# Kernel optimization log

Hardware: AMD Instinct MI355X
Metric: run time of the kernel (lower is better)

The kernel has to match this reference:

```python
import jax, jax.numpy as jnp
import numpy as np

B, D, H, V, T = 64, 1024, 1024, 32000, 20
SOS = 0  # word_to_idx['<SOS>']


def setup_inputs() -> dict:
    key = jax.random.key(0)
    ks = jax.random.split(key, 6)
    s = 0.02
    return {
        "latent_vector": jax.random.normal(ks[0], (B, D), jnp.float32),
        "W_proj": jax.random.normal(ks[1], (H, D), jnp.float32) * s,
        "b_proj": jnp.zeros((H,), jnp.float32),
        "emb": jax.random.normal(ks[2], (V, H), jnp.float32) * s,
        "W_ih": jax.random.normal(ks[3], (3 * H, H), jnp.float32) * s,
        "b_ih": jnp.zeros((3 * H,), jnp.float32),
        "W_hh": jax.random.normal(ks[4], (3 * H, H), jnp.float32) * s,
        "b_hh": jnp.zeros((3 * H,), jnp.float32),
        "W_out": jax.random.normal(ks[5], (V, H), jnp.float32) * s,
        "b_out": jnp.zeros((V,), jnp.float32),
    }


def _gru_cell(x, h, W_ih, b_ih, W_hh, b_hh):
    # PyTorch GRU cell gate math
    gi = x @ W_ih.T + b_ih  # [B, 3H]
    gh = h @ W_hh.T + b_hh  # [B, 3H]
    i_r, i_z, i_n = jnp.split(gi, 3, axis=-1)
    h_r, h_z, h_n = jnp.split(gh, 3, axis=-1)
    r = jax.nn.sigmoid(i_r + h_r)
    z = jax.nn.sigmoid(i_z + h_z)
    n = jnp.tanh(i_n + r * h_n)
    return (1.0 - z) * n + z * h


def reference(latent_vector, W_proj, b_proj, emb, W_ih, b_ih, W_hh, b_hh, W_out, b_out):
    batch = latent_vector.shape[0]
    h = latent_vector @ W_proj.T + b_proj  # init_hidden: [B, H]
    tok0 = jnp.full((batch,), SOS, dtype=jnp.int32)

    def step(carry, _):
        tok, h = carry
        x = emb[tok]                                  # embedding lookup [B, H]
        h = _gru_cell(x, h, W_ih, b_ih, W_hh, b_hh)   # GRU step
        logits = h @ W_out.T + b_out                  # [B, V]
        tok = jnp.argmax(logits, axis=-1).astype(jnp.int32)  # topk(1) greedy
        return (tok, h), tok

    (_, h_final), toks = jax.lax.scan(step, (tok0, h), None, length=T)
    # torch: stack(outputs, dim=1).squeeze() -> [B, T]; hidden -> [1, B, H]
    return toks.T, h_final[None, :, :]
```

## Files before the change

### kernel.cpp

```cpp
#include <hip/hip_runtime.h>
#include <stdint.h>

#define B_ 64
#define D_ 1024
#define H_ 1024
#define V_ 32000
#define T_ 20
#define SOS_ 0

typedef __attribute__((ext_vector_type(8))) __bf16 bf16x8;
typedef __attribute__((ext_vector_type(4))) float f32x4;

__device__ __forceinline__ uint32_t ord_of_float(float x) {
    uint32_t u = __float_as_uint(x);
    return (u & 0x80000000u) ? ~u : (u | 0x80000000u);
}

__device__ __forceinline__ unsigned long long shfl_xor_u64(unsigned long long x, int m) {
    return (unsigned long long)__shfl_xor((long long)x, m, 64);
}

__device__ __forceinline__ void split_bf16(float f, unsigned short* hi, unsigned short* lo) {
    uint32_t u = __float_as_uint(f);
    uint32_t rh = (u + 0x7FFFu + ((u >> 16) & 1u)) >> 16;
    *hi = (unsigned short)rh;
    float fl = f - __uint_as_float(rh << 16);
    uint32_t ul = __float_as_uint(fl);
    uint32_t rl = (ul + 0x7FFFu + ((ul >> 16) & 1u)) >> 16;
    *lo = (unsigned short)rl;
}

__device__ __forceinline__ void gload_lds16(const void* g, void* l) {
    __builtin_amdgcn_global_load_lds(
        (const __attribute__((address_space(1))) void*)g,
        (__attribute__((address_space(3))) void*)l, 16, 0, 0);
}

__global__ __launch_bounds__(256) void k_split_w(const float* __restrict__ src,
    unsigned short* __restrict__ hi, unsigned short* __restrict__ lo, int n4)
{
    int i = blockIdx.x * 256 + threadIdx.x;
    if (i >= n4) return;
    float4 v = ((const float4*)src)[i];
    ushort4 h, l;
    split_bf16(v.x, &h.x, &l.x);
    split_bf16(v.y, &h.y, &l.y);
    split_bf16(v.z, &h.z, &l.z);
    split_bf16(v.w, &h.w, &l.w);
    ((ushort4*)hi)[i] = h;
    ((ushort4*)lo)[i] = l;
}

__global__ __launch_bounds__(256) void k_init_hidden(
    const float* __restrict__ latent, const float* __restrict__ Wp,
    const float* __restrict__ bp, float* __restrict__ h0,
    unsigned short* __restrict__ hhi, unsigned short* __restrict__ hlo)
{
    int gw = (blockIdx.x * 256 + threadIdx.x) >> 6;
    int lane = threadIdx.x & 63;
    int j = gw >> 6;
    int b = gw & 63;
    const float4* a4 = (const float4*)(latent + b * D_);
    const float4* w4 = (const float4*)(Wp + (size_t)j * D_);
    float s = 0.f;
#pragma unroll
    for (int i = 0; i < 4; i++) {
        float4 a = a4[lane + 64 * i];
        float4 w = w4[lane + 64 * i];
        s += a.x * w.x + a.y * w.y + a.z * w.z + a.w * w.w;
    }
#pragma unroll
    for (int off = 32; off; off >>= 1) s += __shfl_down(s, off, 64);
    if (lane == 0) {
        float v = s + bp[j];
        h0[b * H_ + j] = v;
        unsigned short h_, l_;
        split_bf16(v, &h_, &l_);
        hhi[b * H_ + j] = h_;
        hlo[b * H_ + j] = l_;
    }
}

__global__ __launch_bounds__(256) void k_prep_x0(const float* __restrict__ emb,
    unsigned short* __restrict__ xhi, unsigned short* __restrict__ xlo)
{
    int b = blockIdx.x;
    int tid = threadIdx.x;
    float4 v4 = *(const float4*)(emb + (size_t)SOS_ * H_ + tid * 4);
    ushort4 h, l;
    split_bf16(v4.x, &h.x, &l.x);
    split_bf16(v4.y, &h.y, &l.y);
    split_bf16(v4.z, &h.z, &l.z);
    split_bf16(v4.w, &h.w, &l.w);
    *(ushort4*)(xhi + (size_t)b * H_ + tid * 4) = h;
    *(ushort4*)(xlo + (size_t)b * H_ + tid * 4) = l;
}

__global__ __launch_bounds__(256) void k_gates_gemm2(
    const unsigned short* __restrict__ xhi, const unsigned short* __restrict__ xlo,
    const unsigned short* __restrict__ hhi, const unsigned short* __restrict__ hlo,
    const unsigned short* __restrict__ wihh, const unsigned short* __restrict__ wihl,
    const unsigned short* __restrict__ whhh, const unsigned short* __restrict__ whhl,
    float* __restrict__ gbuf)
{
    __shared__ __align__(128) char Bsm[2][16384];
    int tid = threadIdx.x;
    int lane = tid & 63;
    int wv = tid >> 6;
    int blk = blockIdx.x;
    int jt = blk % 48;
    int rest = blk / 48;
    int half = rest & 1;
    int ks = rest >> 1;
    int kbase = ks * 512;
    int row0 = jt * 64;

    const unsigned short* Ahi_g = half ? hhi : xhi;
    const unsigned short* Alo_g = half ? hlo : xlo;
    const unsigned short* Bhi_g = half ? whhh : wihh;
    const unsigned short* Blo_g = half ? whhl : wihl;

    int r0 = wv * 8 + (lane >> 3);
    int r1 = r0 + 32;
    int kslt = (lane & 7) * 16;
    size_t so0 = (size_t)(row0 + r0) * 2048 + (size_t)(kslt ^ ((r0 & 7) << 4));
    size_t so1 = (size_t)(row0 + r1) * 2048 + (size_t)(kslt ^ ((r1 & 7) << 4));

    int mrow = wv * 16 + (lane & 15);
    int koff = (lane >> 4) * 8;
    int kb = koff * 2;

    f32x4 acc[4];
#pragma unroll
    for (int i = 0; i < 4; i++) acc[i] = (f32x4){0.f, 0.f, 0.f, 0.f};

    auto stage = [&](int BUF, int KC) {
        const char* bh = (const char*)Bhi_g + (size_t)KC * 2;
        const char* bl = (const char*)Blo_g + (size_t)KC * 2;
        char* base = Bsm[BUF] + wv * 1024;
        gload_lds16(bh + so0, base);
        gload_lds16(bh + so1, base + 4096);
        gload_lds16(bl + so0, base + 8192);
        gload_lds16(bl + so1, base + 12288);
    };

    int buf = 0;
    stage(0, kbase);
    __syncthreads();
    for (int it = 0; it < 8; ++it) {
        int kc = kbase + it * 64;
        if (it < 7) stage(buf ^ 1, kc + 64);
        const unsigned short* ap = Ahi_g + (size_t)mrow * 1024 + kc + koff;
        const unsigned short* alp = Alo_g + (size_t)mrow * 1024 + kc + koff;
        bf16x8 ah0 = *(const bf16x8*)ap;
        bf16x8 ah1 = *(const bf16x8*)(ap + 32);
        bf16x8 al0 = *(const bf16x8*)alp;
        bf16x8 al1 = *(const bf16x8*)(alp + 32);
        const char* bhp = Bsm[buf];
        const char* blp = Bsm[buf] + 8192;
#pragma unroll
        for (int tv = 0; tv < 4; tv++) {
            int brow = tv * 16 + (lane & 15);
            int swz = (brow & 7) << 4;
            int ro = brow * 128;
            bf16x8 bh0 = *(const bf16x8*)(bhp + ro + (kb ^ swz));
            bf16x8 bh1 = *(const bf16x8*)(bhp + ro + ((kb + 64) ^ swz));
            bf16x8 bl0 = *(const bf16x8*)(blp + ro + (kb ^ swz));
            bf16x8 bl1 = *(const bf16x8*)(blp + ro + ((kb + 64) ^ swz));
            acc[tv] = __builtin_amdgcn_mfma_f32_16x16x32_bf16(ah0, bh0, acc[tv], 0, 0, 0);
            acc[tv] = __builtin_amdgcn_mfma_f32_16x16x32_bf16(ah1, bh1, acc[tv], 0, 0, 0);
            acc[tv] = __builtin_amdgcn_mfma_f32_16x16x32_bf16(al0, bh0, acc[tv], 0, 0, 0);
            acc[tv] = __builtin_amdgcn_mfma_f32_16x16x32_bf16(al1, bh1, acc[tv], 0, 0, 0);
            acc[tv] = __builtin_amdgcn_mfma_f32_16x16x32_bf16(ah0, bl0, acc[tv], 0, 0, 0);
            acc[tv] = __builtin_amdgcn_mfma_f32_16x16x32_bf16(ah1, bl1, acc[tv], 0, 0, 0);
        }
        __syncthreads();
        buf ^= 1;
    }

    int col = lane & 15;
    int quad = lane >> 4;
    float* og = gbuf + (size_t)((ks * 2 + half) * 64) * 3072;
#pragma unroll
    for (int tv = 0; tv < 4; tv++) {
#pragma unroll
        for (int r = 0; r < 4; r++) {
            int b = wv * 16 + quad * 4 + r;
            og[(size_t)b * 3072 + jt * 64 + tv * 16 + col] = acc[tv][r];
        }
    }
}

__global__ __launch_bounds__(256) void k_gru_elem2(
    const float* __restrict__ gbuf, const float* __restrict__ bih,
    const float* __restrict__ bhh, const float* __restrict__ hprev,
    float* __restrict__ hnext, unsigned short* __restrict__ hnhi,
    unsigned short* __restrict__ hnlo)
{
    int idx = blockIdx.x * 256 + threadIdx.x;
    int b = idx >> 10;
    int j = idx & 1023;
    const float* g00 = gbuf + (size_t)b * 3072;
    const float* g01 = gbuf + (size_t)(64 + b) * 3072;
    const float* g10 = gbuf + (size_t)(128 + b) * 3072;
    const float* g11 = gbuf + (size_t)(192 + b) * 3072;
    float ir = g00[j] + g10[j] + bih[j];
    float hr = g01[j] + g11[j] + bhh[j];
    float iz = g00[H_ + j] + g10[H_ + j] + bih[H_ + j];
    float hz = g01[H_ + j] + g11[H_ + j] + bhh[H_ + j];
    float in_ = g00[2 * H_ + j] + g10[2 * H_ + j] + bih[2 * H_ + j];
    float hn = g01[2 * H_ + j] + g11[2 * H_ + j] + bhh[2 * H_ + j];
    float r = 1.f / (1.f + expf(-(ir + hr)));
    float z = 1.f / (1.f + expf(-(iz + hz)));
    float n = tanhf(in_ + r * hn);
    float hp = hprev[idx];
    float v = (1.f - z) * n + z * hp;
    hnext[idx] = v;
    unsigned short h_, l_;
    split_bf16(v, &h_, &l_);
    hnhi[idx] = h_;
    hnlo[idx] = l_;
}

__global__ __launch_bounds__(256) void k_logits_argmax2(
    const unsigned short* __restrict__ hhi, const unsigned short* __restrict__ hlo,
    const unsigned short* __restrict__ wouth, const unsigned short* __restrict__ woutl,
    const float* __restrict__ bout, unsigned long long* __restrict__ partials,
    int nblk)
{
    __shared__ __align__(128) char Bsm[2][16384];
    int tid = threadIdx.x;
    int lane = tid & 63;
    int wv = tid >> 6;
    int row0 = blockIdx.x * 64;

    int r0 = wv * 8 + (lane >> 3);
    int r1 = r0 + 32;
    int kslt = (lane & 7) * 16;
    size_t so0 = (size_t)(row0 + r0) * 2048 + (size_t)(kslt ^ ((r0 & 7) << 4));
    size_t so1 = (size_t)(row0 + r1) * 2048 + (size_t)(kslt ^ ((r1 & 7) << 4));

    int mrow = wv * 16 + (lane & 15);
    int koff = (lane >> 4) * 8;
    int kb = koff * 2;

    f32x4 acc[4];
#pragma unroll
    for (int i = 0; i < 4; i++) acc[i] = (f32x4){0.f, 0.f, 0.f, 0.f};

    auto stage = [&](int BUF, int KC) {
        const char* bh = (const char*)wouth + (size_t)KC * 2;
        const char* bl = (const char*)woutl + (size_t)KC * 2;
        char* base = Bsm[BUF] + wv * 1024;
        gload_lds16(bh + so0, base);
        gload_lds16(bh + so1, base + 4096);
        gload_lds16(bl + so0, base + 8192);
        gload_lds16(bl + so1, base + 12288);
    };

    int buf = 0;
    stage(0, 0);
    __syncthreads();
    for (int it = 0; it < 16; ++it) {
        int kc = it * 64;
        if (it < 15) stage(buf ^ 1, kc + 64);
        const unsigned short* ap = hhi + (size_t)mrow * 1024 + kc + koff;
        const unsigned short* alp = hlo + (size_t)mrow * 1024 + kc + koff;
        bf16x8 ah0 = *(const bf16x8*)ap;
        bf16x8 ah1 = *(const bf16x8*)(ap + 32);
        bf16x8 al0 = *(const bf16x8*)alp;
        bf16x8 al1 = *(const bf16x8*)(alp + 32);
        const char* bhp = Bsm[buf];
        const char* blp = Bsm[buf] + 8192;
#pragma unroll
        for (int tv = 0; tv < 4; tv++) {
            int brow = tv * 16 + (lane & 15);
            int swz = (brow & 7) << 4;
            int ro = brow * 128;
            bf16x8 bh0 = *(const bf16x8*)(bhp + ro + (kb ^ swz));
            bf16x8 bh1 = *(const bf16x8*)(bhp + ro + ((kb + 64) ^ swz));
            bf16x8 bl0 = *(const bf16x8*)(blp + ro + (kb ^ swz));
            bf16x8 bl1 = *(const bf16x8*)(blp + ro + ((kb + 64) ^ swz));
            acc[tv] = __builtin_amdgcn_mfma_f32_16x16x32_bf16(ah0, bh0, acc[tv], 0, 0, 0);
            acc[tv] = __builtin_amdgcn_mfma_f32_16x16x32_bf16(ah1, bh1, acc[tv], 0, 0, 0);
            acc[tv] = __builtin_amdgcn_mfma_f32_16x16x32_bf16(al0, bh0, acc[tv], 0, 0, 0);
            acc[tv] = __builtin_amdgcn_mfma_f32_16x16x32_bf16(al1, bh1, acc[tv], 0, 0, 0);
            acc[tv] = __builtin_amdgcn_mfma_f32_16x16x32_bf16(ah0, bl0, acc[tv], 0, 0, 0);
            acc[tv] = __builtin_amdgcn_mfma_f32_16x16x32_bf16(ah1, bl1, acc[tv], 0, 0, 0);
        }
        __syncthreads();
        buf ^= 1;
    }

    int col = lane & 15;
    int quad = lane >> 4;
    unsigned long long kmax[4] = {0ull, 0ull, 0ull, 0ull};
#pragma unroll
    for (int tv = 0; tv < 4; tv++) {
        int v = row0 + tv * 16 + col;
        float bo = bout[v];
#pragma unroll
        for (int r = 0; r < 4; r++) {
            float lg = acc[tv][r] + bo;
            unsigned long long key = ((unsigned long long)ord_of_float(lg) << 32)
                                   | (unsigned long long)(0x7FFFFFFFu - (uint32_t)v);
            if (key > kmax[r]) kmax[r] = key;
        }
    }
#pragma unroll
    for (int r = 0; r < 4; r++) {
        unsigned long long k = kmax[r];
#pragma unroll
        for (int off = 1; off < 16; off <<= 1) {
            unsigned long long o = shfl_xor_u64(k, off);
            if (o > k) k = o;
        }
        kmax[r] = k;
    }
    if (col == 0) {
#pragma unroll
        for (int r = 0; r < 4; r++) {
            int b = wv * 16 + quad * 4 + r;
            partials[(size_t)b * nblk + blockIdx.x] = kmax[r];
        }
    }
}

__global__ __launch_bounds__(256) void k_token2(
    const unsigned long long* __restrict__ partials, int nblk,
    int* __restrict__ tok, float* __restrict__ out_tokens, int t,
    const float* __restrict__ emb,
    unsigned short* __restrict__ xhi, unsigned short* __restrict__ xlo)
{
    __shared__ int s_tok;
    int b = blockIdx.x;
    int tid = threadIdx.x;
    if (tid < 64) {
        unsigned long long k = 0ull;
        for (int i = tid; i < nblk; i += 64) {
            unsigned long long p = partials[(size_t)b * nblk + i];
            if (p > k) k = p;
        }
#pragma unroll
        for (int off = 32; off; off >>= 1) {
            unsigned long long o = shfl_xor_u64(k, off);
            if (o > k) k = o;
        }
        if (tid == 0) {
            int v = (int)(0x7FFFFFFFu - (uint32_t)(k & 0xFFFFFFFFull));
            tok[b] = v;
            out_tokens[b * T_ + t] = (float)v;
            s_tok = v;
        }
    }
    __syncthreads();
    int row = s_tok;
    float4 v4 = *(const float4*)(emb + (size_t)row * H_ + tid * 4);
    ushort4 h, l;
    split_bf16(v4.x, &h.x, &l.x);
    split_bf16(v4.y, &h.y, &l.y);
    split_bf16(v4.z, &h.z, &l.z);
    split_bf16(v4.w, &h.w, &l.w);
    *(ushort4*)(xhi + (size_t)b * H_ + tid * 4) = h;
    *(ushort4*)(xlo + (size_t)b * H_ + tid * 4) = l;
}

__global__ __launch_bounds__(256) void k_copy_h(const float* __restrict__ h,
                                               float* __restrict__ out)
{
    int i = (blockIdx.x * 256 + threadIdx.x) * 4;
    *(float4*)(out + i) = *(const float4*)(h + i);
}

extern "C" void kernel_launch(void* const* d_in, const int* in_sizes, int n_in,
                              void* d_out, int out_size, void* d_ws, size_t ws_size,
                              hipStream_t stream)
{
    const float* latent = (const float*)d_in[0];
    const float* Wp     = (const float*)d_in[1];
    const float* bp     = (const float*)d_in[2];
    const float* emb    = (const float*)d_in[3];
    const float* Wih    = (const float*)d_in[4];
    const float* bih    = (const float*)d_in[5];
    const float* Whh    = (const float*)d_in[6];
    const float* bhh    = (const float*)d_in[7];
    const float* Wout   = (const float*)d_in[8];
    const float* bout   = (const float*)d_in[9];
    float* out = (float*)d_out;

    char* ws = (char*)d_ws;
    float* h0   = (float*)(ws + 0);
    float* h1   = (float*)(ws + 262144);
    int* tok    = (int*)(ws + 524288);
    unsigned long long* partials = (unsigned long long*)(ws + 525312);
    float* gbuf = (float*)(ws + 787456);
    unsigned short* hhi0 = (unsigned short*)(ws + 3933184);
    unsigned short* hlo0 = (unsigned short*)(ws + 4064256);
    unsigned short* hhi1 = (unsigned short*)(ws + 4195328);
    unsigned short* hlo1 = (unsigned short*)(ws + 4326400);
    unsigned short* xhi  = (unsigned short*)(ws + 4457472);
    unsigned short* xlo  = (unsigned short*)(ws + 4588544);
    unsigned short* wihh = (unsigned short*)(ws + 4719616);
    unsigned short* wihl = (unsigned short*)(ws + 11011072);
    unsigned short* whhh = (unsigned short*)(ws + 17302528);
    unsigned short* whhl = (unsigned short*)(ws + 23593984);
    unsigned short* wouth = (unsigned short*)(ws + 29885440);
    unsigned short* woutl = (unsigned short*)(ws + 95421440);

    const int NBLK = V_ / 64;

    k_split_w<<<3072, 256, 0, stream>>>(Wih, wihh, wihl, 3 * H_ * H_ / 4);
    k_split_w<<<3072, 256, 0, stream>>>(Whh, whhh, whhl, 3 * H_ * H_ / 4);
    k_split_w<<<32000, 256, 0, stream>>>(Wout, wouth, woutl, V_ * H_ / 4);

    k_init_hidden<<<16384, 256, 0, stream>>>(latent, Wp, bp, h0, hhi0, hlo0);
    k_prep_x0<<<64, 256, 0, stream>>>(emb, xhi, xlo);

    float* hp = h0;  unsigned short* hphi = hhi0;  unsigned short* hplo = hlo0;
    float* hn = h1;  unsigned short* hnhi = hhi1;  unsigned short* hnlo = hlo1;
    for (int t = 0; t < T_; t++) {
        k_gates_gemm2<<<192, 256, 0, stream>>>(xhi, xlo, hphi, hplo,
                                               wihh, wihl, whhh, whhl, gbuf);
        k_gru_elem2<<<256, 256, 0, stream>>>(gbuf, bih, bhh, hp, hn, hnhi, hnlo);
        k_logits_argmax2<<<NBLK, 256, 0, stream>>>(hnhi, hnlo, wouth, woutl,
                                                   bout, partials, NBLK);
        k_token2<<<B_, 256, 0, stream>>>(partials, NBLK, tok, out, t, emb, xhi, xlo);
        { float* tf = hp; hp = hn; hn = tf; }
        { unsigned short* ts = hphi; hphi = hnhi; hnhi = ts; }
        { unsigned short* ts = hplo; hplo = hnlo; hnlo = ts; }
    }
    k_copy_h<<<64, 256, 0, stream>>>(hp, out + B_ * T_);
}
```

Before: 1.265 ms.

## Deepen LDS prefetch pipeline and double split-K in gate GEMM

The gate GEMM now splits K four ways instead of two, launching 384 blocks instead of 192. Each block prefetches all four of its 64-wide K chunks into a 4-stage LDS buffer and uses vmcnt waits with raw barriers in place of double buffering. The logits/argmax kernel moves to a 4-deep ring buffer with three stages in flight, issuing each next load after compute and synchronising through explicit s_waitcnt counts. The GRU elementwise kernel sums four partials and the workspace grows to hold the larger gbuf. This aims to hide memory latency and raise occupancy for the bandwidth-bound weight streaming. In exchange it uses more LDS per block and depends on hand-tuned vmcnt counts being correct, and the ring buffer drops the end-of-iteration barrier, which risks overwriting a slot before other waves finish reading it.

Measured after the change: 1.171 ms. -7.4%, faster.

```diff
diff --git a/kernel.cpp b/kernel.cpp
--- a/kernel.cpp
+++ b/kernel.cpp
@@ -103,7 +103,7 @@
     const unsigned short* __restrict__ whhh, const unsigned short* __restrict__ whhl,
     float* __restrict__ gbuf)
 {
-    __shared__ __align__(128) char Bsm[2][16384];
+    __shared__ __align__(128) char Bsm[4][16384];
     int tid = threadIdx.x;
     int lane = tid & 63;
     int wv = tid >> 6;
@@ -112,7 +112,7 @@
     int rest = blk / 48;
     int half = rest & 1;
     int ks = rest >> 1;
-    int kbase = ks * 512;
+    int kbase = ks * 256;
     int row0 = jt * 64;
 
     const unsigned short* Ahi_g = half ? hhi : xhi;
@@ -144,20 +144,24 @@
         gload_lds16(bl + so1, base + 12288);
     };
 
-    int buf = 0;
     stage(0, kbase);
-    __syncthreads();
-    for (int it = 0; it < 8; ++it) {
+    stage(1, kbase + 64);
+    stage(2, kbase + 128);
+    stage(3, kbase + 192);
+
+    for (int it = 0; it < 4; ++it) {
+        asm volatile("s_waitcnt vmcnt(12)" ::: "memory");
+        __builtin_amdgcn_s_barrier();
+        __builtin_amdgcn_sched_barrier(0);
         int kc = kbase + it * 64;
-        if (it < 7) stage(buf ^ 1, kc + 64);
         const unsigned short* ap = Ahi_g + (size_t)mrow * 1024 + kc + koff;
         const unsigned short* alp = Alo_g + (size_t)mrow * 1024 + kc + koff;
         bf16x8 ah0 = *(const bf16x8*)ap;
         bf16x8 ah1 = *(const bf16x8*)(ap + 32);
         bf16x8 al0 = *(const bf16x8*)alp;
         bf16x8 al1 = *(const bf16x8*)(alp + 32);
-        const char* bhp = Bsm[buf];
-        const char* blp = Bsm[buf] + 8192;
+        const char* bhp = Bsm[it];
+        const char* blp = Bsm[it] + 8192;
 #pragma unroll
         for (int tv = 0; tv < 4; tv++) {
             int brow = tv * 16 + (lane & 15);
@@ -174,8 +178,6 @@
             acc[tv] = __builtin_amdgcn_mfma_f32_16x16x32_bf16(ah0, bl0, acc[tv], 0, 0, 0);
             acc[tv] = __builtin_amdgcn_mfma_f32_16x16x32_bf16(ah1, bl1, acc[tv], 0, 0, 0);
         }
-        __syncthreads();
-        buf ^= 1;
     }
 
     int col = lane & 15;
@@ -200,16 +202,17 @@
     int idx = blockIdx.x * 256 + threadIdx.x;
     int b = idx >> 10;
     int j = idx & 1023;
-    const float* g00 = gbuf + (size_t)b * 3072;
-    const float* g01 = gbuf + (size_t)(64 + b) * 3072;
-    const float* g10 = gbuf + (size_t)(128 + b) * 3072;
-    const float* g11 = gbuf + (size_t)(192 + b) * 3072;
-    float ir = g00[j] + g10[j] + bih[j];
-    float hr = g01[j] + g11[j] + bhh[j];
-    float iz = g00[H_ + j] + g10[H_ + j] + bih[H_ + j];
-    float hz = g01[H_ + j] + g11[H_ + j] + bhh[H_ + j];
-    float in_ = g00[2 * H_ + j] + g10[2 * H_ + j] + bih[2 * H_ + j];
-    float hn = g01[2 * H_ + j] + g11[2 * H_ + j] + bhh[2 * H_ + j];
+    float ir = bih[j], hr = bhh[j];
+    float iz = bih[H_ + j], hz = bhh[H_ + j];
+    float in_ = bih[2 * H_ + j], hn = bhh[2 * H_ + j];
+#pragma unroll
+    for (int ks = 0; ks < 4; ks++) {
+        const float* gi = gbuf + (size_t)(ks * 2 * 64 + b) * 3072;
+        const float* gh = gbuf + (size_t)((ks * 2 + 1) * 64 + b) * 3072;
+        ir += gi[j];          hr += gh[j];
+        iz += gi[H_ + j];     hz += gh[H_ + j];
+        in_ += gi[2 * H_ + j]; hn += gh[2 * H_ + j];
+    }
     float r = 1.f / (1.f + expf(-(ir + hr)));
     float z = 1.f / (1.f + expf(-(iz + hz)));
     float n = tanhf(in_ + r * hn);
@@ -228,7 +231,7 @@
     const float* __restrict__ bout, unsigned long long* __restrict__ partials,
     int nblk)
 {
-    __shared__ __align__(128) char Bsm[2][16384];
+    __shared__ __align__(128) char Bsm[4][16384];
     int tid = threadIdx.x;
     int lane = tid & 63;
     int wv = tid >> 6;
@@ -258,20 +261,25 @@
         gload_lds16(bl + so1, base + 12288);
     };
 
-    int buf = 0;
     stage(0, 0);
-    __syncthreads();
+    stage(1, 64);
+    stage(2, 128);
+
     for (int it = 0; it < 16; ++it) {
+        if (it == 0)      asm volatile("s_waitcnt vmcnt(8)"  ::: "memory");
+        else if (it == 1) asm volatile("s_waitcnt vmcnt(12)" ::: "memory");
+        else              asm volatile("s_waitcnt vmcnt(16)" ::: "memory");
+        __builtin_amdgcn_s_barrier();
+        __builtin_amdgcn_sched_barrier(0);
         int kc = it * 64;
-        if (it < 15) stage(buf ^ 1, kc + 64);
         const unsigned short* ap = hhi + (size_t)mrow * 1024 + kc + koff;
         const unsigned short* alp = hlo + (size_t)mrow * 1024 + kc + koff;
         bf16x8 ah0 = *(const bf16x8*)ap;
         bf16x8 ah1 = *(const bf16x8*)(ap + 32);
         bf16x8 al0 = *(const bf16x8*)alp;
         bf16x8 al1 = *(const bf16x8*)(alp + 32);
-        const char* bhp = Bsm[buf];
-        const char* blp = Bsm[buf] + 8192;
+        const char* bhp = Bsm[it & 3];
+        const char* blp = Bsm[it & 3] + 8192;
 #pragma unroll
         for (int tv = 0; tv < 4; tv++) {
             int brow = tv * 16 + (lane & 15);
@@ -288,8 +296,7 @@
             acc[tv] = __builtin_amdgcn_mfma_f32_16x16x32_bf16(ah0, bl0, acc[tv], 0, 0, 0);
             acc[tv] = __builtin_amdgcn_mfma_f32_16x16x32_bf16(ah1, bl1, acc[tv], 0, 0, 0);
         }
-        __syncthreads();
-        buf ^= 1;
+        if (it <= 12) stage((it + 3) & 3, (it + 3) * 64);
     }
 
     int col = lane & 15;
@@ -394,18 +401,18 @@
     int* tok    = (int*)(ws + 524288);
     unsigned long long* partials = (unsigned long long*)(ws + 525312);
     float* gbuf = (float*)(ws + 787456);
-    unsigned short* hhi0 = (unsigned short*)(ws + 3933184);
-    unsigned short* hlo0 = (unsigned short*)(ws + 4064256);
-    unsigned short* hhi1 = (unsigned short*)(ws + 4195328);
-    unsigned short* hlo1 = (unsigned short*)(ws + 4326400);
-    unsigned short* xhi  = (unsigned short*)(ws + 4457472);
-    unsigned short* xlo  = (unsigned short*)(ws + 4588544);
-    unsigned short* wihh = (unsigned short*)(ws + 4719616);
-    unsigned short* wihl = (unsigned short*)(ws + 11011072);
-    unsigned short* whhh = (unsigned short*)(ws + 17302528);
-    unsigned short* whhl = (unsigned short*)(ws + 23593984);
-    unsigned short* wouth = (unsigned short*)(ws + 29885440);
-    unsigned short* woutl = (unsigned short*)(ws + 95421440);
+    unsigned short* hhi0 = (unsigned short*)(ws + 7078912);
+    unsigned short* hlo0 = (unsigned short*)(ws + 7209984);
+    unsigned short* hhi1 = (unsigned short*)(ws + 7341056);
+    unsigned short* hlo1 = (unsigned short*)(ws + 7472128);
+    unsigned short* xhi  = (unsigned short*)(ws + 7603200);
+    unsigned short* xlo  = (unsigned short*)(ws + 7734272);
+    unsigned short* wihh = (unsigned short*)(ws + 7865344);
+    unsigned short* wihl = (unsigned short*)(ws + 14156800);
+    unsigned short* whhh = (unsigned short*)(ws + 20448256);
+    unsigned short* whhl = (unsigned short*)(ws + 26739712);
+    unsigned short* wouth = (unsigned short*)(ws + 33031168);
+    unsigned short* woutl = (unsigned short*)(ws + 98567168);
 
     const int NBLK = V_ / 64;
 
@@ -419,7 +426,7 @@
     float* hp = h0;  unsigned short* hphi = hhi0;  unsigned short* hplo = hlo0;
     float* hn = h1;  unsigned short* hnhi = hhi1;  unsigned short* hnlo = hlo1;
     for (int t = 0; t < T_; t++) {
-        k_gates_gemm2<<<192, 256, 0, stream>>>(xhi, xlo, hphi, hplo,
+        k_gates_gemm2<<<384, 256, 0, stream>>>(xhi, xlo, hphi, hplo,
                                                wihh, wihl, whhh, whhl, gbuf);
         k_gru_elem2<<<256, 256, 0, stream>>>(gbuf, bih, bhh, hp, hn, hnhi, hnlo);
         k_logits_argmax2<<<NBLK, 256, 0, stream>>>(hnhi, hnlo, wouth, woutl,
```
